# Kernel optimization log

Measured on AMD Instinct MI355X. Metric: run time of the kernel, lower is better.

Reference implementation:

```python
import jax, jax.numpy as jnp
import numpy as np

B, N, DV = 32, 1024, 512
L, S, DT = 256, 8, 512
VOCAB = 1024
BAND = 16
LN_EPS = 1e-5


def setup_inputs() -> dict:
    key = jax.random.key(0)
    ks = jax.random.split(key, 12)
    w = lambda k, shp: jax.random.normal(k, shp, dtype=jnp.float32) * 0.02
    return {
        "vis_tokens": jax.random.normal(ks[0], (B, N, DV), dtype=jnp.float32),
        "txt_ctx_ids": jax.random.randint(ks[1], (B, L, S), 0, VOCAB, dtype=jnp.int32),
        "emb_w": w(ks[2], (VOCAB, DT)),        # embedding table, tied with classifier
        "wq": w(ks[3], (DV, DT)),              # q_proj: d_txt -> d_vis
        "wk": w(ks[4], (DV, DV)),
        "wv": w(ks[5], (DV, DV)),
        "wv2t": w(ks[6], (DT, DV)),            # vis2txt: d_vis -> d_txt
        "dw_k": w(ks[7], (DT, 1, 3)),          # depthwise conv1d kernel (O, I/g=1, K)
        "pw_k": w(ks[8], (DT, DT, 1)),         # pointwise conv1d kernel
        "ln_g": jnp.ones((DT,), jnp.float32),
        "ln_b": jnp.zeros((DT,), jnp.float32),
        "dir_alpha": jnp.float32(0.2),
    }


def reference(vis_tokens, txt_ctx_ids, emb_w, wq, wk, wv, wv2t, dw_k, pw_k, ln_g, ln_b, dir_alpha):
    b, n, dv = vis_tokens.shape
    E = emb_w[txt_ctx_ids]                       # [B, L, S, Dt]
    bl = b * E.shape[1]
    x = E.reshape(bl, E.shape[2], DT).transpose(0, 2, 1)  # [B*L, Dt, S]
    dn = ('NCH', 'OIH', 'NCH')
    h = jax.lax.conv_general_dilated(x, dw_k, (1,), 'SAME', dimension_numbers=dn,
                                     feature_group_count=DT)
    y = jax.lax.conv_general_dilated(jax.nn.silu(h), pw_k, (1,), 'SAME', dimension_numbers=dn)
    x = x + y
    m = x.mean(axis=2)                           # [B*L, Dt]
    mu = m.mean(-1, keepdims=True)
    var = ((m - mu) ** 2).mean(-1, keepdims=True)
    q_txt = ((m - mu) * jax.lax.rsqrt(var + LN_EPS) * ln_g + ln_b).reshape(b, -1, DT)  # [B, L, Dt]

    Q = q_txt @ wq.T                             # [B, L, Dv]
    K = vis_tokens @ wk.T                        # [B, N, Dv]
    V = vis_tokens @ wv.T
    logits = jnp.einsum('bld,bnd->bln', Q, K) * (dv ** -0.5)

    # linear centers (torch linspace(0, N-1, L).long() truncates toward zero)
    centers = jnp.linspace(0.0, n - 1, q_txt.shape[1]).astype(jnp.int32)  # [L]
    centers = jnp.broadcast_to(centers[None, :], (b, q_txt.shape[1]))
    idx = jnp.arange(n)[None, None, :]
    signed = (centers[..., None] - idx).astype(jnp.float32)
    logits = logits + dir_alpha * (signed / (BAND + 1e-6))
    keep = jnp.abs(idx - centers[..., None]) <= BAND
    logits = jnp.where(keep, logits, -jnp.inf)

    A = jax.nn.softmax(logits, axis=-1)          # [B, L, N]
    Fv = jnp.einsum('bln,bnd->bld', A, V)        # dropout in source is undefined attr; identity
    H = Fv @ wv2t.T                              # [B, L, Dt]
    cls = H @ emb_w.T                            # tied classifier
    return (cls, H, A)
```

## Files before the change

kernel.cpp:

```cpp
#include <hip/hip_runtime.h>
#include <cmath>

typedef unsigned short u16;
typedef __attribute__((ext_vector_type(8))) short bf16x8;
typedef __attribute__((ext_vector_type(4))) float f32x4;
typedef __attribute__((ext_vector_type(8))) unsigned short u16x8;

#define B_  32
#define N_  1024
#define L_  256
#define S_  8
#define DT_ 512
#define BAND_ 16

__device__ __forceinline__ u16 f2bf(float f) {
  union { float f; unsigned u; } x; x.f = f;
  unsigned r = (x.u + 0x7fffu + ((x.u >> 16) & 1u)) >> 16;
  return (u16)r;
}
__device__ __forceinline__ float bf2f(u16 h) {
  union { unsigned u; float f; } x; x.u = ((unsigned)h) << 16;
  return x.f;
}

#define B1_WAIT(N)                                       \
  asm volatile("s_waitcnt vmcnt(" #N ")" ::: "memory");  \
  __builtin_amdgcn_s_barrier();                          \
  __builtin_amdgcn_sched_barrier(0);
#define B2_BAR()                                         \
  __builtin_amdgcn_sched_barrier(0);                     \
  __builtin_amdgcn_s_barrier();

__global__ __launch_bounds__(256) void cvt_bf16(
    const float* __restrict__ in, u16* __restrict__ out, int n4) {
  int i = blockIdx.x * 256 + threadIdx.x;
  if (i < n4) {
    float4 v = ((const float4*)in)[i];
    ushort4 o;
    o.x = f2bf(v.x); o.y = f2bf(v.y); o.z = f2bf(v.z); o.w = f2bf(v.w);
    ((ushort4*)out)[i] = o;
  }
}

__global__ __launch_bounds__(256) void cvt_weights(
    const float* __restrict__ e, const float* __restrict__ q,
    const float* __restrict__ k, const float* __restrict__ v,
    const float* __restrict__ t, const float* __restrict__ pw,
    u16* __restrict__ eo, u16* __restrict__ qo, u16* __restrict__ kvo,
    u16* __restrict__ to, u16* __restrict__ po) {
  int i = blockIdx.x * 256 + threadIdx.x;
  const float* src; u16* dst; int soff, doff;
  if (i < 131072)      { src = e;  dst = eo;  soff = i;          doff = soff; }
  else if (i < 196608) { src = q;  dst = qo;  soff = i - 131072; doff = soff; }
  else if (i < 262144) { src = k;  dst = kvo; soff = i - 196608; doff = soff; }
  else if (i < 327680) { src = v;  dst = kvo; soff = i - 262144; doff = soff + 65536; }
  else if (i < 393216) { src = t;  dst = to;  soff = i - 327680; doff = soff; }
  else                 { src = pw; dst = po;  soff = i - 393216; doff = soff; }
  float4 vv = ((const float4*)src)[soff];
  ushort4 o;
  o.x = f2bf(vv.x); o.y = f2bf(vv.y); o.z = f2bf(vv.z); o.w = f2bf(vv.w);
  ((ushort4*)dst)[doff] = o;
}

__global__ __launch_bounds__(256) void text_front(
    const int* __restrict__ ids, const float* __restrict__ emb,
    const float* __restrict__ dwk, u16* __restrict__ shm,
    float* __restrict__ mbuf) {
  int bl = blockIdx.x;
  int tid = threadIdx.x;
  __shared__ int sid[S_];
  if (tid < S_) sid[tid] = ids[bl * S_ + tid];
  __syncthreads();
  for (int c = tid; c < DT_; c += 256) {
    float x[S_];
#pragma unroll
    for (int s = 0; s < S_; ++s) x[s] = emb[(size_t)sid[s] * DT_ + c];
    float k0 = dwk[c * 3 + 0], k1 = dwk[c * 3 + 1], k2 = dwk[c * 3 + 2];
    float me = 0.f, sh = 0.f;
#pragma unroll
    for (int s = 0; s < S_; ++s) {
      float xm = (s > 0) ? x[s - 1] : 0.0f;
      float xp = (s < S_ - 1) ? x[s + 1] : 0.0f;
      float h = k0 * xm + k1 * x[s] + k2 * xp;
      float si = h / (1.0f + expf(-h));
      me += x[s];
      sh += si;
    }
    shm[(size_t)bl * DT_ + c] = f2bf(sh * (1.0f / S_));
    mbuf[(size_t)bl * DT_ + c] = me * (1.0f / S_);
  }
}

__global__ __launch_bounds__(512) void gemm_kv_8ph(
    const u16* __restrict__ A, const u16* __restrict__ B,
    u16* __restrict__ Cb, int M, int N, int K) {
  __shared__ u16 As[16384];
  __shared__ u16 Bs[16384];
  const int tid = threadIdx.x;
  const int w = tid >> 6;
  const int lane = tid & 63;
  const int wm = w >> 2, wn = w & 3;

  const int gx = gridDim.x;
  const int bid = blockIdx.y * gx + blockIdx.x;
  const int nwg = gx * gridDim.y;
  const int logical = (bid & 7) * (nwg >> 3) + (bid >> 3);
  const int bm = (logical / gx) << 8;
  const int bn = (logical % gx) << 8;

  const int rowS0 = (w << 5) + (lane >> 2);
  const int rowS1 = rowS0 + 16;
  const int gac = (((lane & 3) ^ ((lane >> 3) & 3)) << 3);
  const u16* AgS0 = A + (size_t)(bm + rowS0) * K + gac;
  const u16* AgS1 = A + (size_t)(bm + rowS1) * K + gac;
  const u16* BgS0 = B + (size_t)(bn + rowS0) * K + gac;
  const u16* BgS1 = B + (size_t)(bn + rowS1) * K + gac;
  const int ldsS0 = (w << 10) + 0;
  const int ldsS1 = (w << 10) + 512;

#define STAGE(step)                                                           \
  {                                                                           \
    const int bufo_ = ((step) & 1) << 13;                                     \
    const int ks_ = (step) << 5;                                              \
    __builtin_amdgcn_global_load_lds(                                         \
        (const __attribute__((address_space(1))) void*)(AgS0 + ks_),          \
        (__attribute__((address_space(3))) void*)(As + bufo_ + ldsS0), 16, 0, 0); \
    __builtin_amdgcn_global_load_lds(                                         \
        (const __attribute__((address_space(1))) void*)(AgS1 + ks_),          \
        (__attribute__((address_space(3))) void*)(As + bufo_ + ldsS1), 16, 0, 0); \
    __builtin_amdgcn_global_load_lds(                                         \
        (const __attribute__((address_space(1))) void*)(BgS0 + ks_),          \
        (__attribute__((address_space(3))) void*)(Bs + bufo_ + ldsS0), 16, 0, 0); \
    __builtin_amdgcn_global_load_lds(                                         \
        (const __attribute__((address_space(1))) void*)(BgS1 + ks_),          \
        (__attribute__((address_space(3))) void*)(Bs + bufo_ + ldsS1), 16, 0, 0); \
  }

  const int kg = lane >> 4;
  int aoff[8], boff[4];
#pragma unroll
  for (int m = 0; m < 8; ++m) {
    const int r = (wm << 7) + (m << 4) + (lane & 15);
    aoff[m] = (r << 5) + ((kg ^ ((r >> 1) & 3)) << 3);
  }
#pragma unroll
  for (int n = 0; n < 4; ++n) {
    const int r = (wn << 6) + (n << 4) + (lane & 15);
    boff[n] = (r << 5) + ((kg ^ ((r >> 1) & 3)) << 3);
  }

  f32x4 acc[8][4];
#pragma unroll
  for (int m = 0; m < 8; ++m)
#pragma unroll
    for (int n = 0; n < 4; ++n) acc[m][n] = (f32x4){0.f, 0.f, 0.f, 0.f};

#define GROUP_BODY(sbuf)                                                      \
  {                                                                           \
    const u16* Ab = As + ((sbuf) << 13);                                      \
    const u16* Bb = Bs + ((sbuf) << 13);                                      \
    bf16x8 af[8], bfr[4];                                                     \
    _Pragma("unroll")                                                         \
    for (int m = 0; m < 8; ++m) af[m] = *(const bf16x8*)(Ab + aoff[m]);       \
    _Pragma("unroll")                                                         \
    for (int n = 0; n < 4; ++n) bfr[n] = *(const bf16x8*)(Bb + boff[n]);      \
    asm volatile("s_waitcnt lgkmcnt(0)" ::: "memory");                        \
    __builtin_amdgcn_sched_barrier(0);                                        \
    __builtin_amdgcn_s_setprio(1);                                            \
    _Pragma("unroll")                                                         \
    for (int m = 0; m < 8; ++m)                                               \
      _Pragma("unroll")                                                       \
      for (int n = 0; n < 4; ++n)                                             \
        acc[m][n] = __builtin_amdgcn_mfma_f32_16x16x32_bf16(                  \
            af[m], bfr[n], acc[m][n], 0, 0, 0);                               \
    __builtin_amdgcn_s_setprio(0);                                            \
  }

  const int nt = K >> 5;
  STAGE(0)
  for (int s = 0; s < nt; ++s) {
    __builtin_amdgcn_s_barrier();
    if (s + 1 < nt) {
      STAGE(s + 1)
      B1_WAIT(4)
    } else {
      B1_WAIT(0)
    }
    GROUP_BODY(s & 1)
  }
#undef GROUP_BODY
#undef STAGE

  const int rb = bm + (wm << 7) + ((lane >> 4) << 2);
  const int cb = bn + (wn << 6) + (lane & 15);
#pragma unroll
  for (int m = 0; m < 8; ++m)
#pragma unroll
    for (int n = 0; n < 4; ++n) {
      const int col = cb + (n << 4);
#pragma unroll
      for (int j = 0; j < 4; ++j) {
        size_t idx = (size_t)(rb + (m << 4) + j) * N + col;
        Cb[idx] = f2bf(acc[m][n][j]);
      }
    }
}

template <bool ACC, bool WF32, bool WBF16>
__global__ __launch_bounds__(256) void gemm_mfma(
    const u16* __restrict__ A, const u16* __restrict__ B,
    float* __restrict__ C, u16* __restrict__ Cb, int M, int N, int K) {
  __shared__ u16 As[8192];
  __shared__ u16 Bs[8192];
  const int tid = threadIdx.x;
  const int w = tid >> 6;
  const int lane = tid & 63;

  const int gx = gridDim.x;
  const int bid = blockIdx.y * gx + blockIdx.x;
  const int nwg = gx * gridDim.y;
  const int logical = (bid & 7) * (nwg >> 3) + (bid >> 3);
  const int bm = (logical / gx) << 7;
  const int bn = (logical % gx) << 7;
  const int wr = w >> 1, wc = w & 1;

  const int r0 = (w << 4) + (lane >> 2);
  const int kc = (lane & 3) << 3;
  const u16* Ag0 = A + (size_t)(bm + r0) * K + kc;
  const u16* Ag1 = Ag0 + (size_t)64 * K;
  const u16* Bg0 = B + (size_t)(bn + r0) * K + kc;
  const u16* Bg1 = Bg0 + (size_t)64 * K;

  int aoff[4], boff[4];
#pragma unroll
  for (int m = 0; m < 4; ++m)
    aoff[m] = (((wr << 6) + (m << 4) + (lane & 15)) << 5) + ((lane >> 4) << 3);
#pragma unroll
  for (int n = 0; n < 4; ++n)
    boff[n] = (((wc << 6) + (n << 4) + (lane & 15)) << 5) + ((lane >> 4) << 3);

  f32x4 acc[4][4];
#pragma unroll
  for (int m = 0; m < 4; ++m)
#pragma unroll
    for (int n = 0; n < 4; ++n) acc[m][n] = (f32x4){0.f, 0.f, 0.f, 0.f};

#define STAGE(buf, kt)                                                        \
  {                                                                           \
    u16* as_ = As + (buf) * 4096 + (w << 9);                                  \
    u16* bs_ = Bs + (buf) * 4096 + (w << 9);                                  \
    __builtin_amdgcn_global_load_lds(                                         \
        (const __attribute__((address_space(1))) void*)(Ag0 + (kt)),          \
        (__attribute__((address_space(3))) void*)as_, 16, 0, 0);              \
    __builtin_amdgcn_global_load_lds(                                         \
        (const __attribute__((address_space(1))) void*)(Ag1 + (kt)),          \
        (__attribute__((address_space(3))) void*)(as_ + 2048), 16, 0, 0);     \
    __builtin_amdgcn_global_load_lds(                                         \
        (const __attribute__((address_space(1))) void*)(Bg0 + (kt)),          \
        (__attribute__((address_space(3))) void*)bs_, 16, 0, 0);              \
    __builtin_amdgcn_global_load_lds(                                         \
        (const __attribute__((address_space(1))) void*)(Bg1 + (kt)),          \
        (__attribute__((address_space(3))) void*)(bs_ + 2048), 16, 0, 0);     \
  }

  const int nt = K >> 5;
  STAGE(0, 0);
  int cur = 0;
  for (int t = 0; t < nt; ++t) {
    if (t + 1 < nt) {
      STAGE(cur ^ 1, (t + 1) << 5);
      B1_WAIT(4)
    } else {
      B1_WAIT(0)
    }
    const u16* Ab = As + cur * 4096;
    const u16* Bb = Bs + cur * 4096;
    bf16x8 af[4], bfr[4];
#pragma unroll
    for (int m = 0; m < 4; ++m) af[m] = *(const bf16x8*)(Ab + aoff[m]);
#pragma unroll
    for (int n = 0; n < 4; ++n) bfr[n] = *(const bf16x8*)(Bb + boff[n]);
#pragma unroll
    for (int m = 0; m < 4; ++m)
#pragma unroll
      for (int n = 0; n < 4; ++n)
        acc[m][n] = __builtin_amdgcn_mfma_f32_16x16x32_bf16(
            af[m], bfr[n], acc[m][n], 0, 0, 0);
    B2_BAR()
    cur ^= 1;
  }
#undef STAGE

  const int rb = bm + (wr << 6) + ((lane >> 4) << 2);
  const int cb = bn + (wc << 6) + (lane & 15);
#pragma unroll
  for (int m = 0; m < 4; ++m)
#pragma unroll
    for (int n = 0; n < 4; ++n) {
      int col = cb + (n << 4);
#pragma unroll
      for (int j = 0; j < 4; ++j) {
        size_t idx = (size_t)(rb + (m << 4) + j) * N + col;
        float v = acc[m][n][j];
        if (ACC) v += C[idx];
        if (WF32) C[idx] = v;
        if (WBF16) Cb[idx] = f2bf(v);
      }
    }
}

template <bool ACC, bool WF32, bool WBF16>
__global__ __launch_bounds__(256) void gemm_n64(
    const u16* __restrict__ A, const u16* __restrict__ B,
    float* __restrict__ C, u16* __restrict__ Cb, int M, int N, int K) {
  __shared__ u16 As[8192];
  __shared__ u16 Bs[4096];
  const int tid = threadIdx.x;
  const int w = tid >> 6;
  const int lane = tid & 63;

  const int gx = gridDim.x;
  const int bid = blockIdx.y * gx + blockIdx.x;
  const int nwg = gx * gridDim.y;
  const int logical = (bid & 7) * (nwg >> 3) + (bid >> 3);
  const int bm = (logical / gx) << 7;
  const int bn = (logical % gx) << 6;

  const int r0 = (w << 4) + (lane >> 2);
  const int kc = (lane & 3) << 3;
  const u16* Ag0 = A + (size_t)(bm + r0) * K + kc;
  const u16* Ag1 = Ag0 + (size_t)64 * K;
  const u16* Bg0 = B + (size_t)(bn + r0) * K + kc;

  int aoff[2], boff[4];
#pragma unroll
  for (int m = 0; m < 2; ++m)
    aoff[m] = (((w << 5) + (m << 4) + (lane & 15)) << 5) + ((lane >> 4) << 3);
#pragma unroll
  for (int n = 0; n < 4; ++n)
    boff[n] = (((n << 4) + (lane & 15)) << 5) + ((lane >> 4) << 3);

  f32x4 acc[2][4];
#pragma unroll
  for (int m = 0; m < 2; ++m)
#pragma unroll
    for (int n = 0; n < 4; ++n) acc[m][n] = (f32x4){0.f, 0.f, 0.f, 0.f};

#define STAGE(buf, kt)                                                        \
  {                                                                           \
    u16* as_ = As + (buf) * 4096 + (w << 9);                                  \
    u16* bs_ = Bs + (buf) * 2048 + (w << 9);                                  \
    __builtin_amdgcn_global_load_lds(                                         \
        (const __attribute__((address_space(1))) void*)(Ag0 + (kt)),          \
        (__attribute__((address_space(3))) void*)as_, 16, 0, 0);              \
    __builtin_amdgcn_global_load_lds(                                         \
        (const __attribute__((address_space(1))) void*)(Ag1 + (kt)),          \
        (__attribute__((address_space(3))) void*)(as_ + 2048), 16, 0, 0);     \
    __builtin_amdgcn_global_load_lds(                                         \
        (const __attribute__((address_space(1))) void*)(Bg0 + (kt)),          \
        (__attribute__((address_space(3))) void*)bs_, 16, 0, 0);              \
  }

  const int nt = K >> 5;
  STAGE(0, 0);
  int cur = 0;
  for (int t = 0; t < nt; ++t) {
    if (t + 1 < nt) {
      STAGE(cur ^ 1, (t + 1) << 5);
      B1_WAIT(3)
    } else {
      B1_WAIT(0)
    }
    const u16* Ab = As + cur * 4096;
    const u16* Bb = Bs + cur * 2048;
    bf16x8 af[2], bfr[4];
#pragma unroll
    for (int m = 0; m < 2; ++m) af[m] = *(const bf16x8*)(Ab + aoff[m]);
#pragma unroll
    for (int n = 0; n < 4; ++n) bfr[n] = *(const bf16x8*)(Bb + boff[n]);
#pragma unroll
    for (int m = 0; m < 2; ++m)
#pragma unroll
      for (int n = 0; n < 4; ++n)
        acc[m][n] = __builtin_amdgcn_mfma_f32_16x16x32_bf16(
            af[m], bfr[n], acc[m][n], 0, 0, 0);
    B2_BAR()
    cur ^= 1;
  }
#undef STAGE

  const int rb = bm + (w << 5) + ((lane >> 4) << 2);
  const int cb = bn + (lane & 15);
#pragma unroll
  for (int m = 0; m < 2; ++m)
#pragma unroll
    for (int n = 0; n < 4; ++n) {
      int col = cb + (n << 4);
#pragma unroll
      for (int j = 0; j < 4; ++j) {
        size_t idx = (size_t)(rb + (m << 4) + j) * N + col;
        float v = acc[m][n][j];
        if (ACC) v += C[idx];
        if (WF32) C[idx] = v;
        if (WBF16) Cb[idx] = f2bf(v);
      }
    }
}

__global__ __launch_bounds__(256) void ln_kernel(
    const float* __restrict__ m, const float* __restrict__ g,
    const float* __restrict__ bta, u16* __restrict__ q) {
  int row = blockIdx.x;
  int tid = threadIdx.x;
  float v0 = m[(size_t)row * 512 + tid];
  float v1 = m[(size_t)row * 512 + 256 + tid];
  __shared__ float red[4], red2[4];
  float s = v0 + v1;
#pragma unroll
  for (int d = 32; d; d >>= 1) s += __shfl_xor(s, d);
  if ((tid & 63) == 0) red[tid >> 6] = s;
  __syncthreads();
  float mu = (red[0] + red[1] + red[2] + red[3]) * (1.0f / 512.0f);
  float d0 = v0 - mu, d1 = v1 - mu;
  float s2 = d0 * d0 + d1 * d1;
#pragma unroll
  for (int d = 32; d; d >>= 1) s2 += __shfl_xor(s2, d);
  if ((tid & 63) == 0) red2[tid >> 6] = s2;
  __syncthreads();
  float var = (red2[0] + red2[1] + red2[2] + red2[3]) * (1.0f / 512.0f);
  float r = rsqrtf(var + 1e-5f);
  q[(size_t)row * 512 + tid] = f2bf(d0 * r * g[tid] + bta[tid]);
  q[(size_t)row * 512 + 256 + tid] = f2bf(d1 * r * g[tid + 256] + bta[tid + 256]);
}

__global__ __launch_bounds__(512) void attn_kernel(
    const u16* __restrict__ Qb, const u16* __restrict__ KV,
    const float* __restrict__ alpha_p, float* __restrict__ A,
    u16* __restrict__ Fv) {
  __shared__ u16 KV_s[96 * 512];
  __shared__ u16 Q_s[16 * 520];
  __shared__ float S_s[16 * 100];

  const int bid = blockIdx.x;
  const int logical = (bid & 7) * 64 + (bid >> 3);
  const int b = logical >> 4, lg = logical & 15;
  const int l0 = lg * 16;
  const int tid = threadIdx.x;
  const int w = tid >> 6, lane = tid & 63;
  const float al = *alpha_p;

  const int c_min = (1023 * l0) / 255;
  const int kb0 = min(max(c_min - BAND_, 0), N_ - 96);

  {
    const size_t rowb = (size_t)(b * N_ + kb0);
    for (int rr = 0; rr < 12; ++rr) {
      const int r = w * 12 + rr;
      const u16* src = KV + (rowb + r) * 1024 + ((lane * 8) ^ ((r & 7) << 3));
      u16* dst = KV_s + r * 512;
      __builtin_amdgcn_global_load_lds(
          (const __attribute__((address_space(1))) void*)src,
          (__attribute__((address_space(3))) void*)dst, 16, 0, 0);
    }
  }
  {
    const int r = tid >> 5;
    const u16* qrow = Qb + (size_t)(b * L_ + l0 + r) * 512;
#pragma unroll
    for (int h = 0; h < 2; ++h) {
      const int ch = (tid & 31) + h * 32;
      u16x8 v = *(const u16x8*)(qrow + ch * 8);
      *(u16x8*)(Q_s + r * 520 + ch * 8) = v;
    }
  }
  __syncthreads();

  if (w < 6) {
    f32x4 acc = {0.f, 0.f, 0.f, 0.f};
    const int arow = (lane & 15) * 520 + ((lane >> 4) << 3);
    const int key = w * 16 + (lane & 15);
    const int swz = (key & 7) << 3;
    for (int ks = 0; ks < 16; ++ks) {
      bf16x8 aq = *(const bf16x8*)(Q_s + arow + ks * 32);
      bf16x8 bk =
          *(const bf16x8*)(KV_s + key * 512 + ((ks * 32 + ((lane >> 4) << 3)) ^ swz));
      acc = __builtin_amdgcn_mfma_f32_16x16x32_bf16(aq, bk, acc, 0, 0, 0);
    }
#pragma unroll
    for (int j = 0; j < 4; ++j)
      S_s[((lane >> 4) * 4 + j) * 100 + w * 16 + (lane & 15)] = acc[j];
  }
  __syncthreads();

  {
    const size_t rowb = (size_t)(b * N_ + kb0);
    for (int rr = 0; rr < 12; ++rr) {
      const int r = w * 12 + rr;
      const u16* src =
          KV + (rowb + r) * 1024 + 512 + ((lane * 8) ^ ((r & 7) << 3));
      u16* dst = KV_s + r * 512;
      __builtin_amdgcn_global_load_lds(
          (const __attribute__((address_space(1))) void*)src,
          (__attribute__((address_space(3))) void*)dst, 16, 0, 0);
    }
  }

#pragma unroll
  for (int rr = 0; rr < 2; ++rr) {
    const int l = 2 * w + rr;
    const int c = (1023 * (l0 + l)) / 255;
    const int g0 = kb0 + lane, g1 = kb0 + 64 + lane;
    const bool v0 = (g0 >= c - BAND_) && (g0 <= c + BAND_);
    const bool v1 = (lane < 32) && (g1 >= c - BAND_) && (g1 <= c + BAND_);
    const float sc = 0.044194173824159216f;
    float x0 = v0 ? S_s[l * 100 + lane] * sc +
                        al * ((float)(c - g0) * (1.0f / 16.000001f))
                  : -INFINITY;
    float x1 = v1 ? S_s[l * 100 + 64 + lane] * sc +
                        al * ((float)(c - g1) * (1.0f / 16.000001f))
                  : -INFINITY;
    float mx = fmaxf(x0, x1);
#pragma unroll
    for (int d = 32; d; d >>= 1) mx = fmaxf(mx, __shfl_xor(mx, d));
    float e0 = v0 ? expf(x0 - mx) : 0.0f;
    float e1 = v1 ? expf(x1 - mx) : 0.0f;
    float sm = e0 + e1;
#pragma unroll
    for (int d = 32; d; d >>= 1) sm += __shfl_xor(sm, d);
    const float inv = 1.0f / sm;
    S_s[l * 100 + lane] = e0 * inv;
    if (lane < 32) S_s[l * 100 + 64 + lane] = e1 * inv;
    const int lo = max(0, c - BAND_), hi = min(N_ - 1, c + BAND_);
    float* Arow = A + (size_t)(b * L_ + l0 + l) * N_;
#pragma unroll
    for (int p4 = 0; p4 < 4; ++p4) {
      const int p = (p4 * 64 + lane) * 4;
      float4 v;
      v.x = (p + 0 >= lo && p + 0 <= hi) ? S_s[l * 100 + p + 0 - kb0] : 0.0f;
      v.y = (p + 1 >= lo && p + 1 <= hi) ? S_s[l * 100 + p + 1 - kb0] : 0.0f;
      v.z = (p + 2 >= lo && p + 2 <= hi) ? S_s[l * 100 + p + 2 - kb0] : 0.0f;
      v.w = (p + 3 >= lo && p + 3 <= hi) ? S_s[l * 100 + p + 3 - kb0] : 0.0f;
      ((float4*)Arow)[p4 * 64 + lane] = v;
    }
  }
  __syncthreads();

#pragma unroll
  for (int rr = 0; rr < 2; ++rr) {
    const int l = 2 * w + rr;
    const int c = (1023 * (l0 + l)) / 255;
    const int jlo = max(0, c - BAND_) - kb0, jhi = min(N_ - 1, c + BAND_) - kb0;
    float acc[8] = {};
    for (int j = jlo; j <= jhi; ++j) {
      const float avj = S_s[l * 100 + j];
      const u16x8 v =
          *(const u16x8*)(KV_s + j * 512 + ((lane * 8) ^ ((j & 7) << 3)));
#pragma unroll
      for (int t = 0; t < 8; ++t) acc[t] += avj * bf2f(v[t]);
    }
    u16x8 fo;
#pragma unroll
    for (int t = 0; t < 8; ++t) fo[t] = f2bf(acc[t]);
    *(u16x8*)(Fv + (size_t)(b * L_ + l0 + l) * 512 + lane * 8) = fo;
  }
}

extern "C" void kernel_launch(void* const* d_in, const int* in_sizes, int n_in,
                              void* d_out, int out_size, void* d_ws,
                              size_t ws_size, hipStream_t stream) {
  const float* vis = (const float*)d_in[0];
  const int* ids = (const int*)d_in[1];
  const float* emb = (const float*)d_in[2];
  const float* wq = (const float*)d_in[3];
  const float* wk = (const float*)d_in[4];
  const float* wvp = (const float*)d_in[5];
  const float* wv2t = (const float*)d_in[6];
  const float* dwk = (const float*)d_in[7];
  const float* pwk = (const float*)d_in[8];
  const float* lng = (const float*)d_in[9];
  const float* lnb = (const float*)d_in[10];
  const float* alpha = (const float*)d_in[11];

  float* out_cls = (float*)d_out;
  float* out_H = out_cls + (size_t)8192 * 1024;
  float* out_A = out_H + (size_t)8192 * 512;

  char* p = (char*)d_ws;
  u16* visb = (u16*)p;              p += (size_t)32768 * 512 * 2;
  u16* KVb  = (u16*)p;              p += (size_t)32768 * 1024 * 2;
  u16* embb = (u16*)p;              p += (size_t)1024 * 512 * 2;
  u16* wqb  = (u16*)p;              p += (size_t)512 * 512 * 2;
  u16* wkvb = (u16*)p;              p += (size_t)1024 * 512 * 2;
  u16* wv2tb= (u16*)p;              p += (size_t)512 * 512 * 2;
  u16* pwkb = (u16*)p;              p += (size_t)512 * 512 * 2;
  u16* shmb = (u16*)p;              p += (size_t)8192 * 512 * 2;
  float* mbuf = (float*)p;          p += (size_t)8192 * 512 * 4;
  u16* qbuf = (u16*)p;              p += (size_t)8192 * 512 * 2;
  u16* Qbf  = (u16*)p;              p += (size_t)8192 * 512 * 2;
  u16* Fvb  = (u16*)p;              p += (size_t)8192 * 512 * 2;
  u16* Hb   = (u16*)p;              p += (size_t)8192 * 512 * 2;

  cvt_bf16<<<16384, 256, 0, stream>>>(vis, visb, 32768 * 512 / 4);
  cvt_weights<<<1792, 256, 0, stream>>>(emb, wq, wk, wvp, wv2t, pwk,
                                        embb, wqb, wkvb, wv2tb, pwkb);

  gemm_kv_8ph<<<dim3(4, 128), 512, 0, stream>>>(
      visb, wkvb, KVb, 32768, 1024, 512);

  text_front<<<8192, 256, 0, stream>>>(ids, emb, dwk, shmb, mbuf);
  gemm_n64<true, true, false><<<dim3(8, 64), 256, 0, stream>>>(
      shmb, pwkb, mbuf, nullptr, 8192, 512, 512);
  ln_kernel<<<8192, 256, 0, stream>>>(mbuf, lng, lnb, qbuf);
  gemm_n64<false, false, true><<<dim3(8, 64), 256, 0, stream>>>(
      qbuf, wqb, nullptr, Qbf, 8192, 512, 512);
  attn_kernel<<<512, 512, 0, stream>>>(Qbf, KVb, alpha, out_A, Fvb);
  gemm_n64<false, true, true><<<dim3(8, 64), 256, 0, stream>>>(
      Fvb, wv2tb, out_H, Hb, 8192, 512, 512);
  gemm_mfma<false, true, false><<<dim3(8, 64), 256, 0, stream>>>(
      Hb, embb, out_cls, nullptr, 8192, 1024, 512);
}
```

Before: 212.8 us.

## Fuse front conversion kernels with text front and shrink KV GEMM tile

Merges the vis conversion, weight conversion and text front-end into one launch that dispatches on block index, which removes two kernel launches and lets the independent work overlap. The KV projection GEMM moves from a 256x256 to a 256x128 tile with 8 waves in a 4x2 layout, which halves the B-tile LDS footprint and doubles the grid. The intent is better occupancy and more workgroups for the 32768x1024 GEMM, at the cost of more A-tile reloads and lower per-wave MFMA density.

```diff
diff --git a/kernel.cpp b/kernel.cpp
--- a/kernel.cpp
+++ b/kernel.cpp
@@ -31,116 +31,111 @@
   __builtin_amdgcn_sched_barrier(0);                     \
   __builtin_amdgcn_s_barrier();
 
-__global__ __launch_bounds__(256) void cvt_bf16(
-    const float* __restrict__ in, u16* __restrict__ out, int n4) {
-  int i = blockIdx.x * 256 + threadIdx.x;
-  if (i < n4) {
-    float4 v = ((const float4*)in)[i];
-    ushort4 o;
-    o.x = f2bf(v.x); o.y = f2bf(v.y); o.z = f2bf(v.z); o.w = f2bf(v.w);
-    ((ushort4*)out)[i] = o;
-  }
-}
-
-__global__ __launch_bounds__(256) void cvt_weights(
+__global__ __launch_bounds__(256) void mega_front(
+    const float* __restrict__ vis, u16* __restrict__ visb,
     const float* __restrict__ e, const float* __restrict__ q,
     const float* __restrict__ k, const float* __restrict__ v,
     const float* __restrict__ t, const float* __restrict__ pw,
     u16* __restrict__ eo, u16* __restrict__ qo, u16* __restrict__ kvo,
-    u16* __restrict__ to, u16* __restrict__ po) {
-  int i = blockIdx.x * 256 + threadIdx.x;
-  const float* src; u16* dst; int soff, doff;
-  if (i < 131072)      { src = e;  dst = eo;  soff = i;          doff = soff; }
-  else if (i < 196608) { src = q;  dst = qo;  soff = i - 131072; doff = soff; }
-  else if (i < 262144) { src = k;  dst = kvo; soff = i - 196608; doff = soff; }
-  else if (i < 327680) { src = v;  dst = kvo; soff = i - 262144; doff = soff + 65536; }
-  else if (i < 393216) { src = t;  dst = to;  soff = i - 327680; doff = soff; }
-  else                 { src = pw; dst = po;  soff = i - 393216; doff = soff; }
-  float4 vv = ((const float4*)src)[soff];
-  ushort4 o;
-  o.x = f2bf(vv.x); o.y = f2bf(vv.y); o.z = f2bf(vv.z); o.w = f2bf(vv.w);
-  ((ushort4*)dst)[doff] = o;
-}
-
-__global__ __launch_bounds__(256) void text_front(
-    const int* __restrict__ ids, const float* __restrict__ emb,
-    const float* __restrict__ dwk, u16* __restrict__ shm,
-    float* __restrict__ mbuf) {
-  int bl = blockIdx.x;
-  int tid = threadIdx.x;
-  __shared__ int sid[S_];
-  if (tid < S_) sid[tid] = ids[bl * S_ + tid];
-  __syncthreads();
-  for (int c = tid; c < DT_; c += 256) {
-    float x[S_];
-#pragma unroll
-    for (int s = 0; s < S_; ++s) x[s] = emb[(size_t)sid[s] * DT_ + c];
-    float k0 = dwk[c * 3 + 0], k1 = dwk[c * 3 + 1], k2 = dwk[c * 3 + 2];
-    float me = 0.f, sh = 0.f;
-#pragma unroll
-    for (int s = 0; s < S_; ++s) {
-      float xm = (s > 0) ? x[s - 1] : 0.0f;
-      float xp = (s < S_ - 1) ? x[s + 1] : 0.0f;
-      float h = k0 * xm + k1 * x[s] + k2 * xp;
-      float si = h / (1.0f + expf(-h));
-      me += x[s];
-      sh += si;
-    }
-    shm[(size_t)bl * DT_ + c] = f2bf(sh * (1.0f / S_));
-    mbuf[(size_t)bl * DT_ + c] = me * (1.0f / S_);
-  }
-}
-
-__global__ __launch_bounds__(512) void gemm_kv_8ph(
+    u16* __restrict__ to, u16* __restrict__ po,
+    const int* __restrict__ ids, const float* __restrict__ dwk,
+    u16* __restrict__ shm, float* __restrict__ mbuf) {
+  const int blk = blockIdx.x;
+  const int tid = threadIdx.x;
+  if (blk < 16384) {
+    int i = blk * 256 + tid;
+    float4 vv = ((const float4*)vis)[i];
+    ushort4 o;
+    o.x = f2bf(vv.x); o.y = f2bf(vv.y); o.z = f2bf(vv.z); o.w = f2bf(vv.w);
+    ((ushort4*)visb)[i] = o;
+  } else if (blk < 18176) {
+    int i = (blk - 16384) * 256 + tid;
+    const float* src; u16* dst; int soff, doff;
+    if (i < 131072)      { src = e;  dst = eo;  soff = i;          doff = soff; }
+    else if (i < 196608) { src = q;  dst = qo;  soff = i - 131072; doff = soff; }
+    else if (i < 262144) { src = k;  dst = kvo; soff = i - 196608; doff = soff; }
+    else if (i < 327680) { src = v;  dst = kvo; soff = i - 262144; doff = soff + 65536; }
+    else if (i < 393216) { src = t;  dst = to;  soff = i - 327680; doff = soff; }
+    else                 { src = pw; dst = po;  soff = i - 393216; doff = soff; }
+    float4 vv = ((const float4*)src)[soff];
+    ushort4 o;
+    o.x = f2bf(vv.x); o.y = f2bf(vv.y); o.z = f2bf(vv.z); o.w = f2bf(vv.w);
+    ((ushort4*)dst)[doff] = o;
+  } else {
+    const int bl = blk - 18176;
+    __shared__ int sid[S_];
+    if (tid < S_) sid[tid] = ids[bl * S_ + tid];
+    __syncthreads();
+    for (int c = tid; c < DT_; c += 256) {
+      float x[S_];
+#pragma unroll
+      for (int s = 0; s < S_; ++s) x[s] = e[(size_t)sid[s] * DT_ + c];
+      float k0 = dwk[c * 3 + 0], k1 = dwk[c * 3 + 1], k2 = dwk[c * 3 + 2];
+      float me = 0.f, sh = 0.f;
+#pragma unroll
+      for (int s = 0; s < S_; ++s) {
+        float xm = (s > 0) ? x[s - 1] : 0.0f;
+        float xp = (s < S_ - 1) ? x[s + 1] : 0.0f;
+        float h = k0 * xm + k1 * x[s] + k2 * xp;
+        float si = h / (1.0f + expf(-h));
+        me += x[s];
+        sh += si;
+      }
+      shm[(size_t)bl * DT_ + c] = f2bf(sh * (1.0f / S_));
+      mbuf[(size_t)bl * DT_ + c] = me * (1.0f / S_);
+    }
+  }
+}
+
+__global__ __launch_bounds__(512) void gemm_kv_v2(
     const u16* __restrict__ A, const u16* __restrict__ B,
     u16* __restrict__ Cb, int M, int N, int K) {
   __shared__ u16 As[16384];
-  __shared__ u16 Bs[16384];
+  __shared__ u16 Bs[8192];
   const int tid = threadIdx.x;
   const int w = tid >> 6;
   const int lane = tid & 63;
-  const int wm = w >> 2, wn = w & 3;
+  const int wm = w >> 1, wn = w & 1;
 
   const int gx = gridDim.x;
   const int bid = blockIdx.y * gx + blockIdx.x;
   const int nwg = gx * gridDim.y;
   const int logical = (bid & 7) * (nwg >> 3) + (bid >> 3);
   const int bm = (logical / gx) << 8;
-  const int bn = (logical % gx) << 8;
-
-  const int rowS0 = (w << 5) + (lane >> 2);
-  const int rowS1 = rowS0 + 16;
+  const int bn = (logical % gx) << 7;
+
+  const int rowA0 = (w << 5) + (lane >> 2);
+  const int rowA1 = rowA0 + 16;
+  const int rowB = (w << 4) + (lane >> 2);
   const int gac = (((lane & 3) ^ ((lane >> 3) & 3)) << 3);
-  const u16* AgS0 = A + (size_t)(bm + rowS0) * K + gac;
-  const u16* AgS1 = A + (size_t)(bm + rowS1) * K + gac;
-  const u16* BgS0 = B + (size_t)(bn + rowS0) * K + gac;
-  const u16* BgS1 = B + (size_t)(bn + rowS1) * K + gac;
-  const int ldsS0 = (w << 10) + 0;
-  const int ldsS1 = (w << 10) + 512;
+  const u16* AgS0 = A + (size_t)(bm + rowA0) * K + gac;
+  const u16* AgS1 = A + (size_t)(bm + rowA1) * K + gac;
+  const u16* BgS = B + (size_t)(bn + rowB) * K + gac;
+  const int ldsA0 = (w << 10);
+  const int ldsA1 = (w << 10) + 512;
+  const int ldsB = (w << 9);
 
 #define STAGE(step)                                                           \
   {                                                                           \
-    const int bufo_ = ((step) & 1) << 13;                                     \
+    const int bufA_ = ((step) & 1) << 13;                                     \
+    const int bufB_ = ((step) & 1) << 12;                                     \
     const int ks_ = (step) << 5;                                              \
     __builtin_amdgcn_global_load_lds(                                         \
         (const __attribute__((address_space(1))) void*)(AgS0 + ks_),          \
-        (__attribute__((address_space(3))) void*)(As + bufo_ + ldsS0), 16, 0, 0); \
+        (__attribute__((address_space(3))) void*)(As + bufA_ + ldsA0), 16, 0, 0); \
     __builtin_amdgcn_global_load_lds(                                         \
         (const __attribute__((address_space(1))) void*)(AgS1 + ks_),          \
-        (__attribute__((address_space(3))) void*)(As + bufo_ + ldsS1), 16, 0, 0); \
-    __builtin_amdgcn_global_load_lds(                                         \
-        (const __attribute__((address_space(1))) void*)(BgS0 + ks_),          \
-        (__attribute__((address_space(3))) void*)(Bs + bufo_ + ldsS0), 16, 0, 0); \
-    __builtin_amdgcn_global_load_lds(                                         \
-        (const __attribute__((address_space(1))) void*)(BgS1 + ks_),          \
-        (__attribute__((address_space(3))) void*)(Bs + bufo_ + ldsS1), 16, 0, 0); \
+        (__attribute__((address_space(3))) void*)(As + bufA_ + ldsA1), 16, 0, 0); \
+    __builtin_amdgcn_global_load_lds(                                         \
+        (const __attribute__((address_space(1))) void*)(BgS + ks_),           \
+        (__attribute__((address_space(3))) void*)(Bs + bufB_ + ldsB), 16, 0, 0); \
   }
 
   const int kg = lane >> 4;
-  int aoff[8], boff[4];
-#pragma unroll
-  for (int m = 0; m < 8; ++m) {
-    const int r = (wm << 7) + (m << 4) + (lane & 15);
+  int aoff[4], boff[4];
+#pragma unroll
+  for (int m = 0; m < 4; ++m) {
+    const int r = (wm << 6) + (m << 4) + (lane & 15);
     aoff[m] = (r << 5) + ((kg ^ ((r >> 1) & 3)) << 3);
   }
 #pragma unroll
@@ -149,26 +144,26 @@
     boff[n] = (r << 5) + ((kg ^ ((r >> 1) & 3)) << 3);
   }
 
-  f32x4 acc[8][4];
-#pragma unroll
-  for (int m = 0; m < 8; ++m)
+  f32x4 acc[4][4];
+#pragma unroll
+  for (int m = 0; m < 4; ++m)
 #pragma unroll
     for (int n = 0; n < 4; ++n) acc[m][n] = (f32x4){0.f, 0.f, 0.f, 0.f};
 
 #define GROUP_BODY(sbuf)                                                      \
   {                                                                           \
     const u16* Ab = As + ((sbuf) << 13);                                      \
-    const u16* Bb = Bs + ((sbuf) << 13);                                      \
-    bf16x8 af[8], bfr[4];                                                     \
+    const u16* Bb = Bs + ((sbuf) << 12);                                      \
+    bf16x8 af[4], bfr[4];                                                     \
     _Pragma("unroll")                                                         \
-    for (int m = 0; m < 8; ++m) af[m] = *(const bf16x8*)(Ab + aoff[m]);       \
+    for (int m = 0; m < 4; ++m) af[m] = *(const bf16x8*)(Ab + aoff[m]);       \
     _Pragma("unroll")                                                         \
     for (int n = 0; n < 4; ++n) bfr[n] = *(const bf16x8*)(Bb + boff[n]);      \
     asm volatile("s_waitcnt lgkmcnt(0)" ::: "memory");                        \
     __builtin_amdgcn_sched_barrier(0);                                        \
     __builtin_amdgcn_s_setprio(1);                                            \
     _Pragma("unroll")                                                         \
-    for (int m = 0; m < 8; ++m)                                               \
+    for (int m = 0; m < 4; ++m)                                               \
       _Pragma("unroll")                                                       \
       for (int n = 0; n < 4; ++n)                                             \
         acc[m][n] = __builtin_amdgcn_mfma_f32_16x16x32_bf16(                  \
@@ -182,7 +177,7 @@
     __builtin_amdgcn_s_barrier();
     if (s + 1 < nt) {
       STAGE(s + 1)
-      B1_WAIT(4)
+      B1_WAIT(3)
     } else {
       B1_WAIT(0)
     }
@@ -191,10 +186,10 @@
 #undef GROUP_BODY
 #undef STAGE
 
-  const int rb = bm + (wm << 7) + ((lane >> 4) << 2);
+  const int rb = bm + (wm << 6) + ((lane >> 4) << 2);
   const int cb = bn + (wn << 6) + (lane & 15);
 #pragma unroll
-  for (int m = 0; m < 8; ++m)
+  for (int m = 0; m < 4; ++m)
 #pragma unroll
     for (int n = 0; n < 4; ++n) {
       const int col = cb + (n << 4);
@@ -600,14 +595,13 @@
   u16* Fvb  = (u16*)p;              p += (size_t)8192 * 512 * 2;
   u16* Hb   = (u16*)p;              p += (size_t)8192 * 512 * 2;
 
-  cvt_bf16<<<16384, 256, 0, stream>>>(vis, visb, 32768 * 512 / 4);
-  cvt_weights<<<1792, 256, 0, stream>>>(emb, wq, wk, wvp, wv2t, pwk,
-                                        embb, wqb, wkvb, wv2tb, pwkb);
-
-  gemm_kv_8ph<<<dim3(4, 128), 512, 0, stream>>>(
+  mega_front<<<26368, 256, 0, stream>>>(
+      vis, visb, emb, wq, wk, wvp, wv2t, pwk,
+      embb, wqb, wkvb, wv2tb, pwkb, ids, dwk, shmb, mbuf);
+
+  gemm_kv_v2<<<dim3(8, 128), 512, 0, stream>>>(
       visb, wkvb, KVb, 32768, 1024, 512);
 
-  text_front<<<8192, 256, 0, stream>>>(ids, emb, dwk, shmb, mbuf);
   gemm_n64<true, true, false><<<dim3(8, 64), 256, 0, stream>>>(
       shmb, pwkb, mbuf, nullptr, 8192, 512, 512);
   ln_kernel<<<8192, 256, 0, stream>>>(mbuf, lng, lnb, qbuf);
```

Result: faster. 199.1 us (-6.4%).
